# Kernel tuning notes

Measured on AMD Instinct MI355X. Metric: run time of the kernel, lower is better.

Reference implementation:

```python
import math
import jax, jax.numpy as jnp
import numpy as np

N = 131072   # flattened batch (agents * timesteps)
D = 4        # input_dim
F = 64       # num_freq_bands
H = 128      # hidden_dim
EPS = 1e-5


def _layer_norm(x, g, b):
    mu = jnp.mean(x, axis=-1, keepdims=True)
    var = jnp.var(x, axis=-1, keepdims=True)
    return (x - mu) * jax.lax.rsqrt(var + EPS) * g + b


def setup_inputs() -> dict:
    key = jax.random.key(0)
    ks = jax.random.split(key, 8)
    fin = 2 * F + 1  # 129
    return {
        "continuous_inputs": jax.random.normal(ks[0], (N, D), dtype=jnp.float32),
        "freqs": jax.random.normal(ks[1], (D, F), dtype=jnp.float32),
        # per-dim MLP ensemble, stacked over D
        "w1": jax.random.normal(ks[2], (D, fin, H), dtype=jnp.float32) * (1.0 / math.sqrt(fin)),
        "b1": jnp.zeros((D, H), dtype=jnp.float32),
        "ln1_g": jnp.ones((D, H), dtype=jnp.float32),
        "ln1_b": jnp.zeros((D, H), dtype=jnp.float32),
        "w2": jax.random.normal(ks[3], (D, H, H), dtype=jnp.float32) * (1.0 / math.sqrt(H)),
        "b2": jnp.zeros((D, H), dtype=jnp.float32),
        # to_out head
        "out_ln_g": jnp.ones((H,), dtype=jnp.float32),
        "out_ln_b": jnp.zeros((H,), dtype=jnp.float32),
        "w3": jax.random.normal(ks[4], (H, H), dtype=jnp.float32) * (1.0 / math.sqrt(H)),
        "b3": jnp.zeros((H,), dtype=jnp.float32),
    }


def reference(continuous_inputs, freqs, w1, b1, ln1_g, ln1_b, w2, b2,
              out_ln_g, out_ln_b, w3, b3):
    # x: [N, D, F] = input[..., None] * freqs * 2*pi
    x = continuous_inputs[..., None] * freqs * (2.0 * math.pi)
    # Fourier features: [N, D, 2F+1]
    feat = jnp.concatenate([jnp.cos(x), jnp.sin(x), continuous_inputs[..., None]], axis=-1)
    # batched per-dim MLP: Linear -> LayerNorm -> ReLU -> Linear, then sum over D
    h = jnp.einsum("ndf,dfh->ndh", feat, w1) + b1          # [N, D, H]
    h = _layer_norm(h, ln1_g, ln1_b)
    h = jax.nn.relu(h)
    h = jnp.einsum("ndh,dhk->ndk", h, w2) + b2             # [N, D, H]
    emb = jnp.sum(h, axis=1)                               # [N, H]
    # to_out: LayerNorm -> ReLU -> Linear
    out = _layer_norm(emb, out_ln_g, out_ln_b)
    out = jax.nn.relu(out)
    return out @ w3 + b3
```

## Files before the change

kernel.cpp:

```cpp
#include <hip/hip_runtime.h>
#include <hip/hip_bf16.h>
#include <math.h>

typedef __bf16 bf16t;
typedef __bf16 bf8v __attribute__((ext_vector_type(8)));
typedef float  f4v  __attribute__((ext_vector_type(4)));
typedef unsigned int u32;
typedef u32 u4v __attribute__((ext_vector_type(4)));

#define DD  4
#define FF  64
#define HH  128
#define FIN 129
#define MT  128

#define AS1 __attribute__((address_space(1)))
#define AS3 __attribute__((address_space(3)))

#define P_FREQS 0
#define P_B1    256
#define P_W1L   768
#define P_G1    1280
#define P_BB1   1792
#define P_B2    2304
#define P_OG    2816
#define P_OB    2944
#define P_B3    3072
#define P_TOT   3200

__device__ __forceinline__ int swz(int row, int k) {
  return row * HH + ((((k >> 3) ^ (row & 7)) << 3) | (k & 7));
}

__device__ __forceinline__ int hperm(int g) {
  return (g & ~31) + (((g & 7) >> 2) << 4) + (((g >> 3) & 3) << 2) + (g & 3);
}

__global__ void prep_weights(const float* __restrict__ w1,
                             const float* __restrict__ w2,
                             const float* __restrict__ w3,
                             bf16t* __restrict__ w1t,
                             bf16t* __restrict__ w2t,
                             bf16t* __restrict__ w3t,
                             float* __restrict__ w1last) {
  int i = blockIdx.x * blockDim.x + threadIdx.x;
  if (i < DD * HH * HH) {
    int d = i >> 14, n = (i >> 7) & 127, g = i & 127;
    w1t[i] = (bf16t)w1[(d * FIN + g) * HH + n];
    w2t[i] = (bf16t)w2[(d * HH + hperm(g)) * HH + n];
  }
  if (i < HH * HH) {
    int n = i >> 7, g = i & 127;
    w3t[i] = (bf16t)w3[hperm(g) * HH + n];
  }
  if (i < DD * HH) {
    int d = i >> 7, n = i & 127;
    w1last[i] = w1[(d * FIN + 128) * HH + n];
  }
}

__device__ __forceinline__ void stage_w_async(const bf16t* __restrict__ w,
                                              bf16t* __restrict__ ldsW,
                                              int tid, int wave) {
  int g0 = (tid & ~15) | ((tid & 15) ^ ((tid >> 4) & 7));
  const bf16t* src = w + g0 * 8;
  bf16t* dst = ldsW + wave * 64 * 8;
  #pragma unroll
  for (int j = 0; j < 8; ++j) {
    __builtin_amdgcn_global_load_lds((const AS1 void*)(src + j * 2048),
                                     (AS3 void*)(dst + j * 2048), 16, 0, 0);
  }
}

__device__ __forceinline__ u32 pack2(float a, float b) {
  union { bf16t h; unsigned short u; } ua, ub;
  ua.h = (bf16t)a; ub.h = (bf16t)b;
  return ((u32)ub.u << 16) | (u32)ua.u;
}

__device__ __forceinline__ void pack_frag(const f4v (&h)[8], bf8v (&bb)[4]) {
  #pragma unroll
  for (int K = 0; K < 4; ++K) {
    u4v wv;
    wv.x = pack2(h[2 * K][0],     h[2 * K][1]);
    wv.y = pack2(h[2 * K][2],     h[2 * K][3]);
    wv.z = pack2(h[2 * K + 1][0], h[2 * K + 1][1]);
    wv.w = pack2(h[2 * K + 1][2], h[2 * K + 1][3]);
    union { u4v w; bf8v v; } cv;
    cv.w = wv;
    bb[K] = cv.v;
  }
}

#define VM_SYNC(N) do {                                        \
    asm volatile("s_waitcnt vmcnt(" #N ")" ::: "memory");      \
    __builtin_amdgcn_s_barrier();                              \
  } while (0)
#define BAR() __builtin_amdgcn_s_barrier()

__launch_bounds__(256, 2)
__global__ void fourier_mlp(
    const float* __restrict__ cont,
    const float* __restrict__ freqs,
    const float* __restrict__ b1,
    const float* __restrict__ ln1g,
    const float* __restrict__ ln1b,
    const float* __restrict__ b2,
    const float* __restrict__ outg,
    const float* __restrict__ outb,
    const float* __restrict__ b3,
    const bf16t* __restrict__ w1t,
    const bf16t* __restrict__ w2t,
    const bf16t* __restrict__ w3t,
    const float* __restrict__ w1last,
    float* __restrict__ out)
{
  __shared__ __align__(16) bf16t ldsW0[HH * HH];
  __shared__ __align__(16) bf16t ldsW1[HH * HH];
  __shared__ __align__(16) float ldsP[P_TOT];

  const int tid  = threadIdx.x;
  const int lane = tid & 63;
  const int wave = tid >> 6;
  const int q    = lane >> 4;
  const int l15  = lane & 15;
  const int rowbase = blockIdx.x * MT;
  const int wrow = wave * 32;

  f4v call[2];
  call[0] = *(const f4v*)&cont[(rowbase + wrow + l15) * DD];
  call[1] = *(const f4v*)&cont[(rowbase + wrow + 16 + l15) * DD];

  stage_w_async(w1t, ldsW0, tid, wave);
  ldsP[P_FREQS + tid] = freqs[tid];
  #pragma unroll
  for (int i = 0; i < 2; ++i) {
    int j = tid + i * 256;
    ldsP[P_B1 + j]  = b1[j];
    ldsP[P_W1L + j] = w1last[j];
    ldsP[P_G1 + j]  = ln1g[j];
    ldsP[P_BB1 + j] = ln1b[j];
    ldsP[P_B2 + j]  = b2[j];
  }
  if (tid < 128) {
    ldsP[P_OG + tid] = outg[tid];
    ldsP[P_OB + tid] = outb[tid];
    ldsP[P_B3 + tid] = b3[tid];
  }

  const f4v fzero = {0.0f, 0.0f, 0.0f, 0.0f};
  f4v emb[2][8];
  #pragma unroll
  for (int g = 0; g < 2; ++g)
    #pragma unroll
    for (int nt = 0; nt < 8; ++nt) emb[g][nt] = fzero;

  __syncthreads();

  for (int d = 0; d < DD; ++d) {
    stage_w_async(w2t + d * HH * HH, ldsW1, tid, wave);

    bf8v fB[2][4];
    #pragma unroll
    for (int g = 0; g < 2; ++g) {
      const float c = call[g][d];
      #pragma unroll
      for (int hf = 0; hf < 2; ++hf) {
        f4v f0 = *(const f4v*)&ldsP[P_FREQS + d * FF + hf * 32 + q * 8];
        f4v f1 = *(const f4v*)&ldsP[P_FREQS + d * FF + hf * 32 + q * 8 + 4];
        #pragma unroll
        for (int u = 0; u < 8; ++u) {
          float fv = (u < 4) ? f0[u] : f1[u - 4];
          float a = c * fv;
          float t = a - floorf(a);
          fB[g][hf][u]     = (bf16t)__builtin_amdgcn_cosf(t);
          fB[g][2 + hf][u] = (bf16t)__builtin_amdgcn_sinf(t);
        }
      }
    }
    VM_SYNC(8);

    f4v acc[2][8];
    #pragma unroll
    for (int g = 0; g < 2; ++g)
      #pragma unroll
      for (int nt = 0; nt < 8; ++nt) acc[g][nt] = fzero;
    #pragma unroll
    for (int K = 0; K < 4; ++K)
      #pragma unroll
      for (int nt = 0; nt < 8; ++nt) {
        bf8v wf = *(const bf8v*)&ldsW0[swz(nt * 16 + l15, K * 32 + q * 8)];
        acc[0][nt] = __builtin_amdgcn_mfma_f32_16x16x32_bf16(wf, fB[0][K], acc[0][nt], 0, 0, 0);
        acc[1][nt] = __builtin_amdgcn_mfma_f32_16x16x32_bf16(wf, fB[1][K], acc[1][nt], 0, 0, 0);
      }
    BAR();

    stage_w_async(d < 3 ? (w1t + (d + 1) * HH * HH) : w3t, ldsW0, tid, wave);

    bf8v bB[2][4];
    #pragma unroll
    for (int g = 0; g < 2; ++g) {
      const float c = call[g][d];
      float s = 0.0f, ss = 0.0f;
      #pragma unroll
      for (int nt = 0; nt < 8; ++nt) {
        f4v b1v = *(const f4v*)&ldsP[P_B1 + d * HH + nt * 16 + q * 4];
        f4v w1l = *(const f4v*)&ldsP[P_W1L + d * HH + nt * 16 + q * 4];
        #pragma unroll
        for (int r = 0; r < 4; ++r) {
          float v = acc[g][nt][r] + b1v[r] + c * w1l[r];
          acc[g][nt][r] = v;
          s += v; ss += v * v;
        }
      }
      s  += __shfl_xor(s, 16);  s  += __shfl_xor(s, 32);
      ss += __shfl_xor(ss, 16); ss += __shfl_xor(ss, 32);
      float mu   = s * (1.0f / 128.0f);
      float var  = ss * (1.0f / 128.0f) - mu * mu;
      float rstd = rsqrtf(var + 1e-5f);
      #pragma unroll
      for (int nt = 0; nt < 8; ++nt) {
        f4v gv = *(const f4v*)&ldsP[P_G1 + d * HH + nt * 16 + q * 4];
        f4v bv = *(const f4v*)&ldsP[P_BB1 + d * HH + nt * 16 + q * 4];
        #pragma unroll
        for (int r = 0; r < 4; ++r) {
          float v = (acc[g][nt][r] - mu) * rstd * gv[r] + bv[r];
          acc[g][nt][r] = fmaxf(v, 0.0f);
        }
      }
      pack_frag(acc[g], bB[g]);
    }
    VM_SYNC(8);

    #pragma unroll
    for (int K = 0; K < 4; ++K)
      #pragma unroll
      for (int nt = 0; nt < 8; ++nt) {
        bf8v wf = *(const bf8v*)&ldsW1[swz(nt * 16 + l15, K * 32 + q * 8)];
        emb[0][nt] = __builtin_amdgcn_mfma_f32_16x16x32_bf16(wf, bB[0][K], emb[0][nt], 0, 0, 0);
        emb[1][nt] = __builtin_amdgcn_mfma_f32_16x16x32_bf16(wf, bB[1][K], emb[1][nt], 0, 0, 0);
      }
    #pragma unroll
    for (int nt = 0; nt < 8; ++nt) {
      f4v b2v = *(const f4v*)&ldsP[P_B2 + d * HH + nt * 16 + q * 4];
      emb[0][nt] += b2v;
      emb[1][nt] += b2v;
    }
    BAR();
  }

  bf8v bB[2][4];
  #pragma unroll
  for (int g = 0; g < 2; ++g) {
    float s = 0.0f, ss = 0.0f;
    #pragma unroll
    for (int nt = 0; nt < 8; ++nt)
      #pragma unroll
      for (int r = 0; r < 4; ++r) {
        float v = emb[g][nt][r];
        s += v; ss += v * v;
      }
    s  += __shfl_xor(s, 16);  s  += __shfl_xor(s, 32);
    ss += __shfl_xor(ss, 16); ss += __shfl_xor(ss, 32);
    float mu   = s * (1.0f / 128.0f);
    float var  = ss * (1.0f / 128.0f) - mu * mu;
    float rstd = rsqrtf(var + 1e-5f);
    #pragma unroll
    for (int nt = 0; nt < 8; ++nt) {
      f4v gv = *(const f4v*)&ldsP[P_OG + nt * 16 + q * 4];
      f4v bv = *(const f4v*)&ldsP[P_OB + nt * 16 + q * 4];
      #pragma unroll
      for (int r = 0; r < 4; ++r) {
        float v = (emb[g][nt][r] - mu) * rstd * gv[r] + bv[r];
        emb[g][nt][r] = fmaxf(v, 0.0f);
      }
    }
    pack_frag(emb[g], bB[g]);
  }
  VM_SYNC(0);

  f4v acc[2][8];
  #pragma unroll
  for (int g = 0; g < 2; ++g)
    #pragma unroll
    for (int nt = 0; nt < 8; ++nt) acc[g][nt] = fzero;
  #pragma unroll
  for (int K = 0; K < 4; ++K)
    #pragma unroll
    for (int nt = 0; nt < 8; ++nt) {
      bf8v wf = *(const bf8v*)&ldsW0[swz(nt * 16 + l15, K * 32 + q * 8)];
      acc[0][nt] = __builtin_amdgcn_mfma_f32_16x16x32_bf16(wf, bB[0][K], acc[0][nt], 0, 0, 0);
      acc[1][nt] = __builtin_amdgcn_mfma_f32_16x16x32_bf16(wf, bB[1][K], acc[1][nt], 0, 0, 0);
    }

  #pragma unroll
  for (int nt = 0; nt < 8; ++nt) {
    f4v b3v = *(const f4v*)&ldsP[P_B3 + nt * 16 + q * 4];
    #pragma unroll
    for (int g = 0; g < 2; ++g) {
      f4v o = acc[g][nt] + b3v;
      *(f4v*)&out[(rowbase + wrow + g * 16 + l15) * HH + nt * 16 + q * 4] = o;
    }
  }
}

extern "C" void kernel_launch(void* const* d_in, const int* in_sizes, int n_in,
                              void* d_out, int out_size, void* d_ws, size_t ws_size,
                              hipStream_t stream) {
  const float* cont  = (const float*)d_in[0];
  const float* freqs = (const float*)d_in[1];
  const float* w1    = (const float*)d_in[2];
  const float* b1    = (const float*)d_in[3];
  const float* ln1g  = (const float*)d_in[4];
  const float* ln1b  = (const float*)d_in[5];
  const float* w2    = (const float*)d_in[6];
  const float* b2    = (const float*)d_in[7];
  const float* outg  = (const float*)d_in[8];
  const float* outb  = (const float*)d_in[9];
  const float* w3    = (const float*)d_in[10];
  const float* b3    = (const float*)d_in[11];
  float* out = (float*)d_out;

  bf16t* w1t = (bf16t*)d_ws;
  bf16t* w2t = w1t + DD * HH * HH;
  bf16t* w3t = w2t + DD * HH * HH;
  float* w1last = (float*)((char*)d_ws + (2 * DD * HH * HH + HH * HH) * sizeof(bf16t));

  prep_weights<<<(DD * HH * HH + 255) / 256, 256, 0, stream>>>(
      w1, w2, w3, w1t, w2t, w3t, w1last);

  int n_rows = in_sizes[0] / DD;
  int grid = n_rows / MT;
  fourier_mlp<<<grid, 256, 0, stream>>>(
      cont, freqs, b1, ln1g, ln1b, b2, outg, outb, b3,
      w1t, w2t, w3t, w1last, out);
}
```

Measured before the change: 169.4 us.

## Software-pipeline Fourier trig and interleave LN epilogue with MFMA per group

```diff
diff --git a/kernel.cpp b/kernel.cpp
--- a/kernel.cpp
+++ b/kernel.cpp
@@ -155,31 +155,69 @@
     #pragma unroll
     for (int nt = 0; nt < 8; ++nt) emb[g][nt] = fzero;
 
-  __syncthreads();
-
-  for (int d = 0; d < DD; ++d) {
-    stage_w_async(w2t + d * HH * HH, ldsW1, tid, wave);
-
-    bf8v fB[2][4];
+  auto trig = [&](int dd, bf8v (&F)[2][4]) {
     #pragma unroll
     for (int g = 0; g < 2; ++g) {
-      const float c = call[g][d];
+      const float c = call[g][dd];
       #pragma unroll
       for (int hf = 0; hf < 2; ++hf) {
-        f4v f0 = *(const f4v*)&ldsP[P_FREQS + d * FF + hf * 32 + q * 8];
-        f4v f1 = *(const f4v*)&ldsP[P_FREQS + d * FF + hf * 32 + q * 8 + 4];
+        f4v f0 = *(const f4v*)&ldsP[P_FREQS + dd * FF + hf * 32 + q * 8];
+        f4v f1 = *(const f4v*)&ldsP[P_FREQS + dd * FF + hf * 32 + q * 8 + 4];
         #pragma unroll
         for (int u = 0; u < 8; ++u) {
           float fv = (u < 4) ? f0[u] : f1[u - 4];
           float a = c * fv;
           float t = a - floorf(a);
-          fB[g][hf][u]     = (bf16t)__builtin_amdgcn_cosf(t);
-          fB[g][2 + hf][u] = (bf16t)__builtin_amdgcn_sinf(t);
+          F[g][hf][u]     = (bf16t)__builtin_amdgcn_cosf(t);
+          F[g][2 + hf][u] = (bf16t)__builtin_amdgcn_sinf(t);
         }
       }
     }
+  };
+
+  auto epilogue = [&](int dd, int gg, f4v (&a8)[8], bf8v (&bb)[4]) {
+    const float c = call[gg][dd];
+    float s = 0.0f, ss = 0.0f;
+    #pragma unroll
+    for (int nt = 0; nt < 8; ++nt) {
+      f4v b1v = *(const f4v*)&ldsP[P_B1 + dd * HH + nt * 16 + q * 4];
+      f4v w1l = *(const f4v*)&ldsP[P_W1L + dd * HH + nt * 16 + q * 4];
+      #pragma unroll
+      for (int r = 0; r < 4; ++r) {
+        float v = a8[nt][r] + b1v[r] + c * w1l[r];
+        a8[nt][r] = v;
+        s += v; ss += v * v;
+      }
+    }
+    s  += __shfl_xor(s, 16);  s  += __shfl_xor(s, 32);
+    ss += __shfl_xor(ss, 16); ss += __shfl_xor(ss, 32);
+    float mu   = s * (1.0f / 128.0f);
+    float var  = ss * (1.0f / 128.0f) - mu * mu;
+    float rstd = rsqrtf(var + 1e-5f);
+    #pragma unroll
+    for (int nt = 0; nt < 8; ++nt) {
+      f4v gv = *(const f4v*)&ldsP[P_G1 + dd * HH + nt * 16 + q * 4];
+      f4v bv = *(const f4v*)&ldsP[P_BB1 + dd * HH + nt * 16 + q * 4];
+      #pragma unroll
+      for (int r = 0; r < 4; ++r) {
+        float v = (a8[nt][r] - mu) * rstd * gv[r] + bv[r];
+        a8[nt][r] = fmaxf(v, 0.0f);
+      }
+    }
+    pack_frag(a8, bb);
+  };
+
+  __syncthreads();
+
+  bf8v fB[2][4];
+  trig(0, fB);
+
+  #pragma unroll
+  for (int d = 0; d < DD; ++d) {
+    stage_w_async(w2t + d * HH * HH, ldsW1, tid, wave);
     VM_SYNC(8);
 
+    __builtin_amdgcn_s_setprio(1);
     f4v acc[2][8];
     #pragma unroll
     for (int g = 0; g < 2; ++g)
@@ -193,53 +231,34 @@
         acc[0][nt] = __builtin_amdgcn_mfma_f32_16x16x32_bf16(wf, fB[0][K], acc[0][nt], 0, 0, 0);
         acc[1][nt] = __builtin_amdgcn_mfma_f32_16x16x32_bf16(wf, fB[1][K], acc[1][nt], 0, 0, 0);
       }
+    bf8v fBn[2][4];
+    if (d < 3) trig(d + 1, fBn);
+    __builtin_amdgcn_s_setprio(0);
     BAR();
 
     stage_w_async(d < 3 ? (w1t + (d + 1) * HH * HH) : w3t, ldsW0, tid, wave);
 
     bf8v bB[2][4];
-    #pragma unroll
-    for (int g = 0; g < 2; ++g) {
-      const float c = call[g][d];
-      float s = 0.0f, ss = 0.0f;
-      #pragma unroll
-      for (int nt = 0; nt < 8; ++nt) {
-        f4v b1v = *(const f4v*)&ldsP[P_B1 + d * HH + nt * 16 + q * 4];
-        f4v w1l = *(const f4v*)&ldsP[P_W1L + d * HH + nt * 16 + q * 4];
-        #pragma unroll
-        for (int r = 0; r < 4; ++r) {
-          float v = acc[g][nt][r] + b1v[r] + c * w1l[r];
-          acc[g][nt][r] = v;
-          s += v; ss += v * v;
-        }
-      }
-      s  += __shfl_xor(s, 16);  s  += __shfl_xor(s, 32);
-      ss += __shfl_xor(ss, 16); ss += __shfl_xor(ss, 32);
-      float mu   = s * (1.0f / 128.0f);
-      float var  = ss * (1.0f / 128.0f) - mu * mu;
-      float rstd = rsqrtf(var + 1e-5f);
-      #pragma unroll
-      for (int nt = 0; nt < 8; ++nt) {
-        f4v gv = *(const f4v*)&ldsP[P_G1 + d * HH + nt * 16 + q * 4];
-        f4v bv = *(const f4v*)&ldsP[P_BB1 + d * HH + nt * 16 + q * 4];
-        #pragma unroll
-        for (int r = 0; r < 4; ++r) {
-          float v = (acc[g][nt][r] - mu) * rstd * gv[r] + bv[r];
-          acc[g][nt][r] = fmaxf(v, 0.0f);
-        }
-      }
-      pack_frag(acc[g], bB[g]);
-    }
+    epilogue(d, 0, acc[0], bB[0]);
     VM_SYNC(8);
 
+    __builtin_amdgcn_s_setprio(1);
     #pragma unroll
     for (int K = 0; K < 4; ++K)
       #pragma unroll
       for (int nt = 0; nt < 8; ++nt) {
         bf8v wf = *(const bf8v*)&ldsW1[swz(nt * 16 + l15, K * 32 + q * 8)];
         emb[0][nt] = __builtin_amdgcn_mfma_f32_16x16x32_bf16(wf, bB[0][K], emb[0][nt], 0, 0, 0);
+      }
+    epilogue(d, 1, acc[1], bB[1]);
+    #pragma unroll
+    for (int K = 0; K < 4; ++K)
+      #pragma unroll
+      for (int nt = 0; nt < 8; ++nt) {
+        bf8v wf = *(const bf8v*)&ldsW1[swz(nt * 16 + l15, K * 32 + q * 8)];
         emb[1][nt] = __builtin_amdgcn_mfma_f32_16x16x32_bf16(wf, bB[1][K], emb[1][nt], 0, 0, 0);
       }
+    __builtin_amdgcn_s_setprio(0);
     #pragma unroll
     for (int nt = 0; nt < 8; ++nt) {
       f4v b2v = *(const f4v*)&ldsP[P_B2 + d * HH + nt * 16 + q * 4];
@@ -247,6 +266,13 @@
       emb[1][nt] += b2v;
     }
     BAR();
+
+    if (d < 3) {
+      #pragma unroll
+      for (int g = 0; g < 2; ++g)
+        #pragma unroll
+        for (int K = 0; K < 4; ++K) fB[g][K] = fBn[g][K];
+    }
   }
 
   bf8v bB[2][4];
```

Measured after the change: 230.5 us. 36.0% more time.
